# Kernel optimization log

Hardware: AMD Instinct MI355X
Metric: run time of the kernel (lower is better)

The kernel has to match this reference:

```python
import jax, jax.numpy as jnp
import numpy as np

B, C, H, W = 8, 256, 128, 128
NUM_HEADS = 8
EPS = 1e-6


def setup_inputs() -> dict:
    key = jax.random.key(0)
    ks = jax.random.split(key, 7)
    s = 1.0 / np.sqrt(C)
    return {
        "x": jax.random.normal(ks[0], (B, C, H, W), dtype=jnp.float32),
        "Wq": jax.random.normal(ks[1], (C, C), dtype=jnp.float32) * s,
        "bq": jax.random.normal(ks[2], (C,), dtype=jnp.float32) * 0.01,
        "Wk": jax.random.normal(ks[3], (C, C), dtype=jnp.float32) * s,
        "bk": jax.random.normal(ks[4], (C,), dtype=jnp.float32) * 0.01,
        "Wv": jax.random.normal(ks[5], (C, C), dtype=jnp.float32) * s,
        "bv": jax.random.normal(ks[6], (C,), dtype=jnp.float32) * 0.01,
    }


def reference(x, Wq, bq, Wk, bk, Wv, bv):
    b, c_full, h_sp, w_sp = x.shape
    p = NUM_HEADS
    c = c_full // p  # per-head channels
    n = h_sp * w_sp  # spatial tokens

    def proj(Wm, bm):
        # 1x1 conv == channel-mixing linear: out[b,o,h,w] = sum_c W[o,c]*x[b,c,h,w] + b[o]
        return jnp.einsum('bchw,oc->bohw', x, Wm) + bm[None, :, None, None]

    q = jax.nn.softplus(proj(Wq, bq)).reshape(b, p, c, n).transpose(0, 1, 3, 2)  # [b,p,n,c]
    k = jax.nn.softplus(proj(Wk, bk)).reshape(b, p, c, n)                        # [b,p,c,n]
    v = proj(Wv, bv).reshape(b, p, c, n)                                         # [b,p,c,n]

    # KV accumulation: [b,p,c_k,c_v] (small)
    kv = jnp.einsum('bpmn,bpcn->bpmc', k, v)
    # normalization: 1 / (q . (sum_n k + eps))
    norm = 1.0 / jnp.einsum('bpnc,bpc->bpn', q, jnp.sum(k, axis=-1) + EPS)
    out = jnp.einsum('bpnm,bpmc,bpn->bpcn', q, kv, norm)  # [b,p,c,n]
    return out.reshape(b, c_full, h_sp, w_sp)
```

## Files before the change

### kernel.cpp

```cpp
#include <hip/hip_runtime.h>
#include <hip/hip_bf16.h>
#include <math.h>

#define BATCH 8
#define CFULL 256
#define HEADS 8
#define CH 32
#define NTOK 16384
#define TN 64
#define EPS 1e-6f

#define SWZ(tok) ((((tok) & 7) << 3) ^ ((((tok) >> 3) & 3) << 6))

typedef __bf16 bf16x8 __attribute__((ext_vector_type(8)));
typedef float f32x4 __attribute__((ext_vector_type(4)));
typedef float f32x16 __attribute__((ext_vector_type(16)));
typedef float fvec4 __attribute__((ext_vector_type(4)));
typedef unsigned short ushort8v __attribute__((ext_vector_type(8)));
typedef int int4v __attribute__((ext_vector_type(4)));

__device__ __forceinline__ unsigned short bf16bits(float f) {
    return __builtin_bit_cast(unsigned short, (__bf16)f);
}
__device__ __forceinline__ float softplus_f(float x) {
    return fmaxf(x, 0.0f) + __logf(1.0f + __expf(-fabsf(x)));
}

__device__ __forceinline__ void quad_transpose(fvec4& a, int lane) {
    const bool o1 = lane & 1, o2 = lane & 2;
    float s1 = o1 ? a.x : a.y; float g1 = __shfl_xor(s1, 1);
    float s2 = o1 ? a.z : a.w; float g2 = __shfl_xor(s2, 1);
    a.x = o1 ? g1 : a.x;  a.y = o1 ? a.y : g1;
    a.z = o1 ? g2 : a.z;  a.w = o1 ? a.w : g2;
    float s3 = o2 ? a.x : a.z; float g3 = __shfl_xor(s3, 2);
    float s4 = o2 ? a.y : a.w; float g4 = __shfl_xor(s4, 2);
    a.x = o2 ? g3 : a.x;  a.z = o2 ? a.z : g3;
    a.y = o2 ? g4 : a.y;  a.w = o2 ? a.w : g4;
}

template <int NW>
__device__ __forceinline__ void stage_x(const float* __restrict__ xb, int n0,
                                        unsigned short* xs, int wv, int lane) {
    const int q4 = lane & 3;
    const int t0 = (lane >> 2) << 2;
    constexpr int G = 64 / NW;
    #pragma unroll
    for (int g = 0; g < G; ++g) {
        const int c0 = wv * (G * 4) + g * 4;
        fvec4 a = __builtin_nontemporal_load(
            (const fvec4*)(xb + (size_t)(c0 + q4) * NTOK + n0 + t0));
        quad_transpose(a, lane);
        ushort4 pk;
        pk.x = bf16bits(a.x); pk.y = bf16bits(a.y);
        pk.z = bf16bits(a.z); pk.w = bf16bits(a.w);
        *(ushort4*)&xs[lane * CFULL + (c0 ^ SWZ(lane))] = pk;
    }
}

template <int NW>
__device__ __forceinline__ void stage_tile(const unsigned short* __restrict__ xTb,
                                           int n0, unsigned short* xs, int wv, int lane) {
    constexpr int R = 64 / NW;
    const unsigned short* src = xTb + (size_t)(n0 + wv * R) * CFULL + lane * 8;
    unsigned short* dst = &xs[wv * R * CFULL];
    #pragma unroll
    for (int i = 0; i < R / 2; ++i) {
        __builtin_amdgcn_global_load_lds(
            (const __attribute__((address_space(1))) unsigned int*)(src + i * 512),
            (__attribute__((address_space(3))) unsigned int*)(dst + i * 512),
            16, 0, 0);
    }
}

__global__ void prep_w(const float* __restrict__ Wq, const float* __restrict__ Wk,
                       const float* __restrict__ Wv, unsigned short* __restrict__ dst)
{
    const int i = blockIdx.x * 256 + threadIdx.x;
    const float* src = (i < 65536) ? Wq : ((i < 131072) ? Wk : Wv);
    dst[i] = bf16bits(src[i & 65535]);
}

__global__ __launch_bounds__(256, 4)
void xpose(const float* __restrict__ x, unsigned short* __restrict__ xT)
{
    __shared__ __align__(16) unsigned short xs[TN * CFULL];
    const int tid = threadIdx.x;
    const int lane = tid & 63;
    const int wv = tid >> 6;
    const int b = blockIdx.x >> 8;
    const int n0 = (blockIdx.x & 255) * TN;

    stage_x<4>(x + (size_t)b * CFULL * NTOK, n0, xs, wv, lane);
    __syncthreads();
    int4v* dst = (int4v*)(xT + ((size_t)b * NTOK + n0) * CFULL);
    const int4v* src = (const int4v*)xs;
    #pragma unroll
    for (int i = 0; i < 8; ++i)
        __builtin_nontemporal_store(src[i * 256 + tid], &dst[i * 256 + tid]);
}

__global__ __launch_bounds__(512)
void k1_kv(const unsigned short* __restrict__ xT,
           const unsigned short* __restrict__ Wk,
           const unsigned short* __restrict__ Wv,
           const float* __restrict__ bk, const float* __restrict__ bv,
           float* __restrict__ kvpart, float* __restrict__ kspart,
           int bpb, int ntiles)
{
    __shared__ __align__(16) unsigned short xs[TN * CFULL];
    __shared__ __align__(16) unsigned short ks[CFULL * TN];

    const int tid = threadIdx.x;
    const int lane = tid & 63;
    const int wv = tid >> 6;
    const int l15 = lane & 15;
    const int lhi = lane >> 4;
    const int bid = blockIdx.x;
    const int b = bid / bpb;
    const int blk = bid % bpb;
    const unsigned short* xTb = xT + (size_t)b * NTOK * CFULL;

    float bkr[2], bvr[2];
    #pragma unroll
    for (int of = 0; of < 2; ++of) {
        bkr[of] = bk[wv * 32 + of * 16 + l15];
        bvr[of] = bv[wv * 32 + of * 16 + l15];
    }

    f32x16 kvacc = {};
    float ksum[2] = {0.f, 0.f};

    for (int t = 0; t < ntiles; ++t) {
        const int n0 = (blk * ntiles + t) * TN;
        __syncthreads();
        stage_tile<8>(xTb, n0, xs, wv, lane);
        __syncthreads();

        #pragma unroll
        for (int tfh = 0; tfh < 2; ++tfh) {
            f32x4 acc[2][2] = {};
            #pragma unroll
            for (int kk = 0; kk < 8; ++kk) {
                const int ch0 = kk * 32 + lhi * 8;
                bf16x8 af[2], bfr[2];
                #pragma unroll
                for (int tf = 0; tf < 2; ++tf) {
                    const int tok = (tfh * 2 + tf) * 16 + l15;
                    af[tf] = *(const bf16x8*)&xs[tok * CFULL + (ch0 ^ SWZ(tok))];
                }
                #pragma unroll
                for (int of = 0; of < 2; ++of) {
                    const int och = wv * 32 + of * 16 + l15;
                    bfr[of] = *(const bf16x8*)&Wk[och * CFULL + ch0];
                }
                #pragma unroll
                for (int tf = 0; tf < 2; ++tf)
                    #pragma unroll
                    for (int of = 0; of < 2; ++of)
                        acc[tf][of] = __builtin_amdgcn_mfma_f32_16x16x32_bf16(af[tf], bfr[of], acc[tf][of], 0, 0, 0);
            }
            #pragma unroll
            for (int tf = 0; tf < 2; ++tf) {
                #pragma unroll
                for (int of = 0; of < 2; ++of) {
                    const int och = wv * 32 + of * 16 + l15;
                    const float bias = bkr[of];
                    float v0 = softplus_f(acc[tf][of][0] + bias);
                    float v1 = softplus_f(acc[tf][of][1] + bias);
                    float v2 = softplus_f(acc[tf][of][2] + bias);
                    float v3 = softplus_f(acc[tf][of][3] + bias);
                    ksum[of] += v0 + v1 + v2 + v3;
                    ushort4 pk;
                    pk.x = bf16bits(v0); pk.y = bf16bits(v1);
                    pk.z = bf16bits(v2); pk.w = bf16bits(v3);
                    const int tok0 = (tfh * 2 + tf) * 16 + lhi * 4;
                    *(ushort4*)&ks[och * TN + (tok0 ^ ((och & 7) << 3))] = pk;
                }
            }
        }

        ushort4 vpk[4][2];
        #pragma unroll
        for (int tfh = 0; tfh < 2; ++tfh) {
            f32x4 acc[2][2] = {};
            #pragma unroll
            for (int kk = 0; kk < 8; ++kk) {
                const int ch0 = kk * 32 + lhi * 8;
                bf16x8 af[2], bfr[2];
                #pragma unroll
                for (int tf = 0; tf < 2; ++tf) {
                    const int tok = (tfh * 2 + tf) * 16 + l15;
                    af[tf] = *(const bf16x8*)&xs[tok * CFULL + (ch0 ^ SWZ(tok))];
                }
                #pragma unroll
                for (int of = 0; of < 2; ++of) {
                    const int och = wv * 32 + of * 16 + l15;
                    bfr[of] = *(const bf16x8*)&Wv[och * CFULL + ch0];
                }
                #pragma unroll
                for (int tf = 0; tf < 2; ++tf)
                    #pragma unroll
                    for (int of = 0; of < 2; ++of)
                        acc[tf][of] = __builtin_amdgcn_mfma_f32_16x16x32_bf16(af[tf], bfr[of], acc[tf][of], 0, 0, 0);
            }
            #pragma unroll
            for (int tf = 0; tf < 2; ++tf)
                #pragma unroll
                for (int of = 0; of < 2; ++of) {
                    const float bias = bvr[of];
                    vpk[tfh * 2 + tf][of].x = bf16bits(acc[tf][of][0] + bias);
                    vpk[tfh * 2 + tf][of].y = bf16bits(acc[tf][of][1] + bias);
                    vpk[tfh * 2 + tf][of].z = bf16bits(acc[tf][of][2] + bias);
                    vpk[tfh * 2 + tf][of].w = bf16bits(acc[tf][of][3] + bias);
                }
        }
        __syncthreads();
        #pragma unroll
        for (int tf = 0; tf < 4; ++tf)
            #pragma unroll
            for (int of = 0; of < 2; ++of) {
                const int och = wv * 32 + of * 16 + l15;
                const int tok0 = tf * 16 + lhi * 4;
                *(ushort4*)&xs[och * TN + (tok0 ^ ((och & 7) << 3))] = vpk[tf][of];
            }

        {
            const int l31 = lane & 31;
            const int tb = (lane >> 5) * 8;
            const int row = wv * 32 + l31;
            #pragma unroll
            for (int ts = 0; ts < 4; ++ts) {
                const int sw = (ts * 16 + tb) ^ ((row & 7) << 3);
                bf16x8 ak = *(const bf16x8*)&ks[row * TN + sw];
                bf16x8 av = *(const bf16x8*)&xs[row * TN + sw];
                kvacc = __builtin_amdgcn_mfma_f32_32x32x16_bf16(ak, av, kvacc, 0, 0, 0);
            }
        }
    }

    #pragma unroll
    for (int of = 0; of < 2; ++of) {
        float v = ksum[of];
        v += __shfl_xor(v, 16);
        v += __shfl_xor(v, 32);
        if (lhi == 0) kspart[bid * CFULL + wv * 32 + of * 16 + l15] = v;
    }
    {
        float* kvp = kvpart + ((size_t)bid << 13);
        const int l31 = lane & 31;
        const int hi = lane >> 5;
        #pragma unroll
        for (int q = 0; q < 4; ++q) {
            const int m0 = 8 * q + 4 * hi;
            f32x4 s;
            s[0] = kvacc[4 * q + 0]; s[1] = kvacc[4 * q + 1];
            s[2] = kvacc[4 * q + 2]; s[3] = kvacc[4 * q + 3];
            *(f32x4*)&kvp[wv * 1024 + l31 * 32 + m0] = s;
        }
    }
}

__global__ __launch_bounds__(256)
void k1r(const float* __restrict__ kvpart, const float* __restrict__ kspart,
         unsigned short* __restrict__ kvT, float* __restrict__ kse, int bpb)
{
    const int o = blockIdx.x * 256 + threadIdx.x;
    const int b = o >> 13;
    const int r = o & 8191;
    float s = 0.f;
    for (int j = 0; j < bpb; ++j)
        s += kvpart[((size_t)(b * bpb + j) << 13) + r];
    kvT[o] = bf16bits(s);
    if (blockIdx.x < BATCH) {
        const int bb = blockIdx.x;
        float t = 0.f;
        for (int j = 0; j < bpb; ++j)
            t += kspart[(bb * bpb + j) * CFULL + threadIdx.x];
        kse[bb * CFULL + threadIdx.x] = t + EPS;
    }
}

__global__ __launch_bounds__(512)
void k2_out(const unsigned short* __restrict__ xT,
            const unsigned short* __restrict__ Wq,
            const float* __restrict__ bq,
            const unsigned short* __restrict__ kvT, const float* __restrict__ ksef,
            float* __restrict__ outp)
{
    __shared__ __align__(16) unsigned short xs[TN * CFULL];
    __shared__ float kse[CFULL];
    __shared__ float normls[HEADS][TN];

    const int tid = threadIdx.x;
    const int lane = tid & 63;
    const int wv = tid >> 6;
    const int l15 = lane & 15;
    const int lhi = lane >> 4;
    const int b = blockIdx.x >> 8;
    const int blk = blockIdx.x & 255;
    const int n0 = blk * TN;
    float* ob = outp + (size_t)b * CFULL * NTOK;

    stage_tile<8>(xT + (size_t)b * NTOK * CFULL, n0, xs, wv, lane);

    if (tid < CFULL) kse[tid] = ksef[b * CFULL + tid];

    float bq0[2][4];
    #pragma unroll
    for (int of = 0; of < 2; ++of) {
        const int och0 = wv * 32 + of * 16 + lhi * 4;
        #pragma unroll
        for (int r = 0; r < 4; ++r) bq0[of][r] = bq[och0 + r];
    }

    __syncthreads();

    ushort4 qpk[2][4];
    {
        f32x4 acc[2][4] = {};
        #pragma unroll
        for (int kk = 0; kk < 8; ++kk) {
            const int ch0 = kk * 32 + lhi * 8;
            bf16x8 aw[2], bx[4];
            #pragma unroll
            for (int of = 0; of < 2; ++of)
                aw[of] = *(const bf16x8*)&Wq[(wv * 32 + of * 16 + l15) * CFULL + ch0];
            #pragma unroll
            for (int nf = 0; nf < 4; ++nf) {
                const int tok = nf * 16 + l15;
                bx[nf] = *(const bf16x8*)&xs[tok * CFULL + (ch0 ^ SWZ(tok))];
            }
            #pragma unroll
            for (int of = 0; of < 2; ++of)
                #pragma unroll
                for (int nf = 0; nf < 4; ++nf)
                    acc[of][nf] = __builtin_amdgcn_mfma_f32_16x16x32_bf16(aw[of], bx[nf], acc[of][nf], 0, 0, 0);
        }
        #pragma unroll
        for (int of = 0; of < 2; ++of) {
            #pragma unroll
            for (int nf = 0; nf < 4; ++nf) {
                qpk[of][nf].x = bf16bits(softplus_f(acc[of][nf][0] + bq0[of][0]));
                qpk[of][nf].y = bf16bits(softplus_f(acc[of][nf][1] + bq0[of][1]));
                qpk[of][nf].z = bf16bits(softplus_f(acc[of][nf][2] + bq0[of][2]));
                qpk[of][nf].w = bf16bits(softplus_f(acc[of][nf][3] + bq0[of][3]));
            }
        }
    }
    __syncthreads();
    #pragma unroll
    for (int of = 0; of < 2; ++of)
        #pragma unroll
        for (int nf = 0; nf < 4; ++nf) {
            const int tok = nf * 16 + l15;
            const int och0 = wv * 32 + of * 16 + lhi * 4;
            *(ushort4*)&xs[tok * CFULL + (och0 ^ SWZ(tok))] = qpk[of][nf];
        }

    {
        float d = 0.f;
        #pragma unroll
        for (int mg = 0; mg < 4; ++mg) {
            bf16x8 qv = *(const bf16x8*)&xs[lane * CFULL + ((wv * 32 + mg * 8) ^ SWZ(lane))];
            #pragma unroll
            for (int j = 0; j < 8; ++j)
                d += (float)qv[j] * kse[wv * 32 + mg * 8 + j];
        }
        normls[wv][lane] = 1.0f / d;
    }

    bf16x8 bh[2];
    {
        const int base = (b * HEADS + wv) << 10;
        #pragma unroll
        for (int hf = 0; hf < 2; ++hf)
            bh[hf] = *(const bf16x8*)&kvT[base + (hf * 16 + l15) * 32 + lhi * 8];
    }

    #pragma unroll
    for (int nf = 0; nf < 4; ++nf) {
        const int tok = nf * 16 + l15;
        bf16x8 af = *(const bf16x8*)&xs[tok * CFULL + ((wv * 32 + lhi * 8) ^ SWZ(tok))];
        f32x4 oA = {}, oB = {};
        oA = __builtin_amdgcn_mfma_f32_16x16x32_bf16(af, bh[0], oA, 0, 0, 0);
        oB = __builtin_amdgcn_mfma_f32_16x16x32_bf16(af, bh[1], oB, 0, 0, 0);
        const int tb = nf * 16 + lhi * 4;
        f32x4 sA, sB;
        sA[0] = oA[0] * normls[wv][tb + 0]; sA[1] = oA[1] * normls[wv][tb + 1];
        sA[2] = oA[2] * normls[wv][tb + 2]; sA[3] = oA[3] * normls[wv][tb + 3];
        sB[0] = oB[0] * normls[wv][tb + 0]; sB[1] = oB[1] * normls[wv][tb + 1];
        sB[2] = oB[2] * normls[wv][tb + 2]; sB[3] = oB[3] * normls[wv][tb + 3];
        __builtin_nontemporal_store(sA, (f32x4*)&ob[(size_t)(wv * 32 + l15) * NTOK + n0 + tb]);
        __builtin_nontemporal_store(sB, (f32x4*)&ob[(size_t)(wv * 32 + 16 + l15) * NTOK + n0 + tb]);
    }
}

extern "C" void kernel_launch(void* const* d_in, const int* in_sizes, int n_in,
                              void* d_out, int out_size, void* d_ws, size_t ws_size,
                              hipStream_t stream)
{
    const float* x  = (const float*)d_in[0];
    const float* Wq = (const float*)d_in[1];
    const float* bq = (const float*)d_in[2];
    const float* Wk = (const float*)d_in[3];
    const float* bk = (const float*)d_in[4];
    const float* Wv = (const float*)d_in[5];
    const float* bv = (const float*)d_in[6];
    float* out = (float*)d_out;

    unsigned char* ws = (unsigned char*)d_ws;
    unsigned short* wbf = (unsigned short*)ws;
    unsigned short* kvT = (unsigned short*)(ws + 393216);
    float* kse = (float*)(ws + 524288);

    const size_t xT_sz = (size_t)BATCH * NTOK * CFULL * 2;

    int bpb = 64;
    size_t ksp_off = 532480;
    size_t kvp_off = ksp_off + (size_t)BATCH * bpb * CFULL * 4;
    size_t kvp_sz  = (size_t)BATCH * bpb * 8192 * 4;
    if (ws_size < kvp_off + kvp_sz + xT_sz) {
        bpb = 16;
        kvp_off = ksp_off + (size_t)BATCH * bpb * CFULL * 4;
        kvp_sz  = (size_t)BATCH * bpb * 8192 * 4;
    }
    float* kspart = (float*)(ws + ksp_off);
    float* kvpart = (float*)(ws + kvp_off);
    unsigned short* xT = (unsigned short*)(ws + kvp_off + kvp_sz);
    const int ntiles = NTOK / TN / bpb;

    hipLaunchKernelGGL(prep_w, dim3(768), dim3(256), 0, stream, Wq, Wk, Wv, wbf);
    hipLaunchKernelGGL(xpose, dim3(BATCH * 256), dim3(256), 0, stream, x, xT);
    hipLaunchKernelGGL(k1_kv, dim3(BATCH * bpb), dim3(512), 0, stream,
                       xT, wbf + 65536, wbf + 2 * 65536, bk, bv,
                       kvpart, kspart, bpb, ntiles);
    hipLaunchKernelGGL(k1r, dim3(256), dim3(256), 0, stream,
                       kvpart, kspart, kvT, kse, bpb);
    hipLaunchKernelGGL(k2_out, dim3(BATCH * 256), dim3(512), 0, stream,
                       xT, wbf, bq, kvT, kse, out);
}
```

Before: 223.2 us.

## Switch K/V projection to 32x32x16 MFMA with weight-as-A operand layout

```diff
diff --git a/kernel.cpp b/kernel.cpp
--- a/kernel.cpp
+++ b/kernel.cpp
@@ -109,26 +109,29 @@
 {
     __shared__ __align__(16) unsigned short xs[TN * CFULL];
     __shared__ __align__(16) unsigned short ks[CFULL * TN];
+    __shared__ float bkl[CFULL];
+    __shared__ float bvl[CFULL];
 
     const int tid = threadIdx.x;
     const int lane = tid & 63;
     const int wv = tid >> 6;
-    const int l15 = lane & 15;
-    const int lhi = lane >> 4;
+    const int l31 = lane & 31;
+    const int hi = lane >> 5;
     const int bid = blockIdx.x;
     const int b = bid / bpb;
     const int blk = bid % bpb;
     const unsigned short* xTb = xT + (size_t)b * NTOK * CFULL;
 
-    float bkr[2], bvr[2];
-    #pragma unroll
-    for (int of = 0; of < 2; ++of) {
-        bkr[of] = bk[wv * 32 + of * 16 + l15];
-        bvr[of] = bv[wv * 32 + of * 16 + l15];
-    }
+    if (tid < CFULL) { bkl[tid] = bk[tid]; bvl[tid] = bv[tid]; }
+
+    const int row = wv * 32 + l31;
+    const unsigned short* WkR = Wk + (size_t)row * CFULL + hi * 8;
+    const unsigned short* WvR = Wv + (size_t)row * CFULL + hi * 8;
+    const int swzB = SWZ(l31);
+    const int rowswz = (row & 7) << 3;
 
     f32x16 kvacc = {};
-    float ksum[2] = {0.f, 0.f};
+    float ksum = 0.f;
 
     for (int t = 0; t < ntiles; ++t) {
         const int n0 = (blk * ntiles + t) * TN;
@@ -136,119 +139,62 @@
         stage_tile<8>(xTb, n0, xs, wv, lane);
         __syncthreads();
 
-        #pragma unroll
-        for (int tfh = 0; tfh < 2; ++tfh) {
-            f32x4 acc[2][2] = {};
-            #pragma unroll
-            for (int kk = 0; kk < 8; ++kk) {
-                const int ch0 = kk * 32 + lhi * 8;
-                bf16x8 af[2], bfr[2];
-                #pragma unroll
-                for (int tf = 0; tf < 2; ++tf) {
-                    const int tok = (tfh * 2 + tf) * 16 + l15;
-                    af[tf] = *(const bf16x8*)&xs[tok * CFULL + (ch0 ^ SWZ(tok))];
-                }
-                #pragma unroll
-                for (int of = 0; of < 2; ++of) {
-                    const int och = wv * 32 + of * 16 + l15;
-                    bfr[of] = *(const bf16x8*)&Wk[och * CFULL + ch0];
-                }
-                #pragma unroll
-                for (int tf = 0; tf < 2; ++tf)
-                    #pragma unroll
-                    for (int of = 0; of < 2; ++of)
-                        acc[tf][of] = __builtin_amdgcn_mfma_f32_16x16x32_bf16(af[tf], bfr[of], acc[tf][of], 0, 0, 0);
+        {
+            f32x16 a0 = {}, a1 = {};
+            #pragma unroll
+            for (int kk = 0; kk < 16; ++kk) {
+                bf16x8 aw = *(const bf16x8*)&WkR[kk * 16];
+                const int ch = (kk * 16 + hi * 8) ^ swzB;
+                bf16x8 b0 = *(const bf16x8*)&xs[l31 * CFULL + ch];
+                bf16x8 b1 = *(const bf16x8*)&xs[(32 + l31) * CFULL + ch];
+                a0 = __builtin_amdgcn_mfma_f32_32x32x16_bf16(aw, b0, a0, 0, 0, 0);
+                a1 = __builtin_amdgcn_mfma_f32_32x32x16_bf16(aw, b1, a1, 0, 0, 0);
             }
             #pragma unroll
-            for (int tf = 0; tf < 2; ++tf) {
-                #pragma unroll
-                for (int of = 0; of < 2; ++of) {
-                    const int och = wv * 32 + of * 16 + l15;
-                    const float bias = bkr[of];
-                    float v0 = softplus_f(acc[tf][of][0] + bias);
-                    float v1 = softplus_f(acc[tf][of][1] + bias);
-                    float v2 = softplus_f(acc[tf][of][2] + bias);
-                    float v3 = softplus_f(acc[tf][of][3] + bias);
-                    ksum[of] += v0 + v1 + v2 + v3;
-                    ushort4 pk;
-                    pk.x = bf16bits(v0); pk.y = bf16bits(v1);
-                    pk.z = bf16bits(v2); pk.w = bf16bits(v3);
-                    const int tok0 = (tfh * 2 + tf) * 16 + lhi * 4;
-                    *(ushort4*)&ks[och * TN + (tok0 ^ ((och & 7) << 3))] = pk;
-                }
+            for (int r = 0; r < 16; ++r) {
+                const int och = wv * 32 + (r & 3) + 8 * (r >> 2) + 4 * hi;
+                const float bias = bkl[och];
+                const int swz = (och & 7) << 3;
+                ks[och * TN + (l31 ^ swz)]        = bf16bits(softplus_f(a0[r] + bias));
+                ks[och * TN + ((32 + l31) ^ swz)] = bf16bits(softplus_f(a1[r] + bias));
             }
         }
 
-        ushort4 vpk[4][2];
-        #pragma unroll
-        for (int tfh = 0; tfh < 2; ++tfh) {
-            f32x4 acc[2][2] = {};
-            #pragma unroll
-            for (int kk = 0; kk < 8; ++kk) {
-                const int ch0 = kk * 32 + lhi * 8;
-                bf16x8 af[2], bfr[2];
-                #pragma unroll
-                for (int tf = 0; tf < 2; ++tf) {
-                    const int tok = (tfh * 2 + tf) * 16 + l15;
-                    af[tf] = *(const bf16x8*)&xs[tok * CFULL + (ch0 ^ SWZ(tok))];
-                }
-                #pragma unroll
-                for (int of = 0; of < 2; ++of) {
-                    const int och = wv * 32 + of * 16 + l15;
-                    bfr[of] = *(const bf16x8*)&Wv[och * CFULL + ch0];
-                }
-                #pragma unroll
-                for (int tf = 0; tf < 2; ++tf)
-                    #pragma unroll
-                    for (int of = 0; of < 2; ++of)
-                        acc[tf][of] = __builtin_amdgcn_mfma_f32_16x16x32_bf16(af[tf], bfr[of], acc[tf][of], 0, 0, 0);
-            }
-            #pragma unroll
-            for (int tf = 0; tf < 2; ++tf)
-                #pragma unroll
-                for (int of = 0; of < 2; ++of) {
-                    const float bias = bvr[of];
-                    vpk[tfh * 2 + tf][of].x = bf16bits(acc[tf][of][0] + bias);
-                    vpk[tfh * 2 + tf][of].y = bf16bits(acc[tf][of][1] + bias);
-                    vpk[tfh * 2 + tf][of].z = bf16bits(acc[tf][of][2] + bias);
-                    vpk[tfh * 2 + tf][of].w = bf16bits(acc[tf][of][3] + bias);
-                }
+        f32x16 c0 = {}, c1 = {};
+        #pragma unroll
+        for (int kk = 0; kk < 16; ++kk) {
+            bf16x8 aw = *(const bf16x8*)&WvR[kk * 16];
+            const int ch = (kk * 16 + hi * 8) ^ swzB;
+            bf16x8 b0 = *(const bf16x8*)&xs[l31 * CFULL + ch];
+            bf16x8 b1 = *(const bf16x8*)&xs[(32 + l31) * CFULL + ch];
+            c0 = __builtin_amdgcn_mfma_f32_32x32x16_bf16(aw, b0, c0, 0, 0, 0);
+            c1 = __builtin_amdgcn_mfma_f32_32x32x16_bf16(aw, b1, c1, 0, 0, 0);
         }
         __syncthreads();
         #pragma unroll
-        for (int tf = 0; tf < 4; ++tf)
-            #pragma unroll
-            for (int of = 0; of < 2; ++of) {
-                const int och = wv * 32 + of * 16 + l15;
-                const int tok0 = tf * 16 + lhi * 4;
-                *(ushort4*)&xs[och * TN + (tok0 ^ ((och & 7) << 3))] = vpk[tf][of];
-            }
-
-        {
-            const int l31 = lane & 31;
-            const int tb = (lane >> 5) * 8;
-            const int row = wv * 32 + l31;
-            #pragma unroll
-            for (int ts = 0; ts < 4; ++ts) {
-                const int sw = (ts * 16 + tb) ^ ((row & 7) << 3);
-                bf16x8 ak = *(const bf16x8*)&ks[row * TN + sw];
-                bf16x8 av = *(const bf16x8*)&xs[row * TN + sw];
-                kvacc = __builtin_amdgcn_mfma_f32_32x32x16_bf16(ak, av, kvacc, 0, 0, 0);
-            }
-        }
-    }
-
-    #pragma unroll
-    for (int of = 0; of < 2; ++of) {
-        float v = ksum[of];
-        v += __shfl_xor(v, 16);
-        v += __shfl_xor(v, 32);
-        if (lhi == 0) kspart[bid * CFULL + wv * 32 + of * 16 + l15] = v;
-    }
+        for (int r = 0; r < 16; ++r) {
+            const int och = wv * 32 + (r & 3) + 8 * (r >> 2) + 4 * hi;
+            const float bias = bvl[och];
+            const int swz = (och & 7) << 3;
+            xs[och * TN + (l31 ^ swz)]        = bf16bits(c0[r] + bias);
+            xs[och * TN + ((32 + l31) ^ swz)] = bf16bits(c1[r] + bias);
+        }
+
+        #pragma unroll
+        for (int ts = 0; ts < 4; ++ts) {
+            const int sw = (ts * 16 + hi * 8) ^ rowswz;
+            bf16x8 ak = *(const bf16x8*)&ks[row * TN + sw];
+            bf16x8 av = *(const bf16x8*)&xs[row * TN + sw];
+            kvacc = __builtin_amdgcn_mfma_f32_32x32x16_bf16(ak, av, kvacc, 0, 0, 0);
+            #pragma unroll
+            for (int j = 0; j < 8; ++j) ksum += (float)ak[j];
+        }
+    }
+
+    ksum += __shfl_xor(ksum, 32);
+    if (hi == 0) kspart[bid * CFULL + row] = ksum;
     {
         float* kvp = kvpart + ((size_t)bid << 13);
-        const int l31 = lane & 31;
-        const int hi = lane >> 5;
         #pragma unroll
         for (int q = 0; q < 4; ++q) {
             const int m0 = 8 * q + 4 * hi;
```

After: 249.2 us. 1.12x slower.
